# Performance work log

Measured on AMD Instinct MI355X. Metric: run time of the kernel, lower is better.

Reference implementation:

```python
import jax, jax.numpy as jnp
import numpy as np

B, S, D, V, K, H, L, U = 256, 50, 32, 10000, 16, 64, 2, 32
NORM = 0.01


def setup_inputs() -> dict:
    key = jax.random.key(0)
    ks = iter(jax.random.split(key, 64))
    r = lambda *sh: jax.random.normal(next(ks), sh, dtype=jnp.float32) * 0.05
    inp = {
        'x1': r(B, U), 'z1': r(B, S, D), 'x2': r(B, U), 'z2': r(B, S, D),
        'embd': r(V, D),
        'dec_w1': r(D, H), 'dec_b1': r(H), 'dec_w2': r(H, D), 'dec_b2': r(D),
        'i_wih': r(3 * D, D), 'i_whh': r(3 * D, D), 'i_bih': r(3 * D), 'i_bhh': r(3 * D),
        'c_wih': r(3 * D, D), 'c_whh': r(3 * D, D), 'c_bih': r(3 * D), 'c_bhh': r(3 * D),
        'im_w1': r(D, D), 'im_b1': r(D), 'im_w2': r(D, D), 'im_b2': r(D),
        'cm_w1': r(D, D), 'cm_b1': r(D), 'cm_w2': r(D, D), 'cm_b2': r(D),
        'hw1': r(L, D, K * K), 'hb1': r(L, K * K), 'hw2': r(L, D, K * K), 'hb2': r(L, K * K),
        'lin_w': r(L, U, K), 'lin_b': r(L, K), 'lout_w': r(L, K, U), 'lout_b': r(L, U),
        'sample_num': B, 'trigger_seq_length': 30,
    }
    return inp


def _gru(x, wih, whh, bih, bhh):
    # PyTorch GRU, batch_first, h0 = 0; gate order (r, z, n)
    gi = jnp.einsum('bsd,ed->bse', x, wih) + bih  # [B,S,3D]

    def step(h, gi_t):
        gh = h @ whh.T + bhh
        gir, giz, gin = jnp.split(gi_t, 3, axis=-1)
        ghr, ghz, ghn = jnp.split(gh, 3, axis=-1)
        rr = jax.nn.sigmoid(gir + ghr)
        zz = jax.nn.sigmoid(giz + ghz)
        nn = jnp.tanh(gin + rr * ghn)
        h = (1.0 - zz) * nn + zz * h
        return h, h

    h0 = jnp.zeros((x.shape[0], whh.shape[1]), x.dtype)
    _, hs = jax.lax.scan(step, h0, jnp.swapaxes(gi, 0, 1))
    return jnp.swapaxes(hs, 0, 1)  # [B,S,D]


def _forward(x1, z1, x2, z2, embd, dec_w1, dec_b1, dec_w2, dec_b2,
             i_wih, i_whh, i_bih, i_bhh, c_wih, c_whh, c_bih, c_bhh,
             im_w1, im_b1, im_w2, im_b2, cm_w1, cm_b1, cm_w2, cm_b2,
             hw1, hb1, hw2, hb2, lin_w, lin_b, lout_w, lout_b,
             sample_num, trigger_seq_length):
    # --- VQVAE.find_nearest: cdist + argmin + gather (index path has no grad) ---
    q = jax.lax.stop_gradient(z1)
    t = jax.lax.stop_gradient(embd)
    # ||q - t||^2 expanded; argmin over sqrt == argmin over squared dist
    d2 = ((q * q).sum(-1)[:, :, None]
          - 2.0 * jnp.einsum('bsd,vd->bsv', q, t)
          + (t * t).sum(-1)[None, None, :])  # [B,S,V]
    idx = jnp.argmin(d2, axis=2)  # [B,S]
    z_emb = embd[idx]  # [B,S,D], gradient flows into embd via gather

    # --- VQVAE.decode ---
    h = jax.nn.leaky_relu(z_emb @ dec_w1 + dec_b1, negative_slope=0.1)
    z_recon = h @ dec_w2 + dec_b2  # [B,S,D]

    total_loss = jnp.mean((z2 - jax.lax.stop_gradient(z_emb)) ** 2)

    # --- item branch: GRU -> pick trigger step -> MLP (tanh, linear) ---
    hs = _gru(z_recon, i_wih, i_whh, i_bih, i_bhh)
    u1 = hs[:, trigger_seq_length, :]
    z1f = jnp.tanh(u1 @ im_w1 + im_b1) @ im_w2 + im_b2  # [B,D]

    # --- category branch ---
    hs = _gru(z2, c_wih, c_whh, c_bih, c_bhh)
    u2 = hs[:, trigger_seq_length, :]
    z2f = jnp.tanh(u2 @ cm_w1 + cm_b1) @ cm_w2 + cm_b2  # [B,D]

    # --- hypernetwork layers (activations in self.modules are never applied) ---
    out = x1
    for i in range(L):
        iw = (z1f @ hw1[i] + hb1[i]).reshape(sample_num, K, K)
        cw = (z2f @ hw2[i] + hb2[i]).reshape(sample_num, K, K)
        w = jnp.clip(iw, -NORM, NORM) + cw  # [B,K,K]
        out = out @ lin_w[i] + lin_b[i]  # [B,K]
        out = jnp.einsum('bk,bkj->bj', out, w)  # bmm
        out = out @ lout_w[i] + lout_b[i]  # [B,U]
    return out, total_loss


def reference(x1, z1, x2, z2, embd, dec_w1, dec_b1, dec_w2, dec_b2,
              i_wih, i_whh, i_bih, i_bhh, c_wih, c_whh, c_bih, c_bhh,
              im_w1, im_b1, im_w2, im_b2, cm_w1, cm_b1, cm_w2, cm_b2,
              hw1, hb1, hw2, hb2, lin_w, lin_b, lout_w, lout_b,
              sample_num, trigger_seq_length):
    return _forward(x1, z1, x2, z2, embd, dec_w1, dec_b1, dec_w2, dec_b2,
                    i_wih, i_whh, i_bih, i_bhh, c_wih, c_whh, c_bih, c_bhh,
                    im_w1, im_b1, im_w2, im_b2, cm_w1, cm_b1, cm_w2, cm_b2,
                    hw1, hb1, hw2, hb2, lin_w, lin_b, lout_w, lout_b,
                    sample_num, trigger_seq_length)
```

## Files before the change

kernel.cpp:

```cpp
#include <hip/hip_runtime.h>
#include <math.h>

#define B 256
#define S 50
#define D 32
#define V 10000
#define VPAD 10240
#define KK 16
#define HH 64
#define LL 2
#define UU 32
#define TT 30
#define NROWS (B*S)
#define NORMC 0.01f
#define CH 256
#define NSLICE 8
#define SLICE_V 1280
#define VQ_RB 128

typedef __attribute__((ext_vector_type(8))) short bf16x8;
typedef __attribute__((ext_vector_type(4))) float f32x4;

__device__ __forceinline__ float sigmoidf_(float x) { return 1.0f / (1.0f + expf(-x)); }

__device__ __forceinline__ unsigned short f2bf(float x) {
    union { float f; unsigned int u; } a; a.f = x;
    unsigned int u = a.u;
    return (unsigned short)((u + 0x7FFFu + ((u >> 16) & 1u)) >> 16);
}
__device__ __forceinline__ float bf2f(unsigned short h) {
    union { unsigned int u; float f; } a; a.u = ((unsigned int)h) << 16; return a.f;
}

__device__ __forceinline__ void gld16(void* lds, const void* g) {
    __builtin_amdgcn_global_load_lds(
        (const __attribute__((address_space(1))) unsigned int*)g,
        (__attribute__((address_space(3))) unsigned int*)lds, 16, 0, 0);
}
__device__ __forceinline__ void gld4(void* lds, const void* g) {
    __builtin_amdgcn_global_load_lds(
        (const __attribute__((address_space(1))) unsigned int*)g,
        (__attribute__((address_space(3))) unsigned int*)lds, 4, 0, 0);
}

__global__ __launch_bounds__(256) void k_prep(const float* __restrict__ embd,
                                              const float* __restrict__ z1,
                                              unsigned short* __restrict__ Eh, unsigned short* __restrict__ El,
                                              unsigned short* __restrict__ Qh, unsigned short* __restrict__ Ql,
                                              float* __restrict__ tn, float* __restrict__ loss_sum) {
    int gid = blockIdx.x * 256 + threadIdx.x;
    if (gid == 0) loss_sum[0] = 0.f;
    if (gid >= VPAD * 4 + 4 * NROWS) return;
    int isRow = (gid >= VPAD * 4);
    if (!isRow) {
        int item = gid >> 2, qd = gid & 3;
        unsigned short* dh = Eh + (size_t)item * D + qd * 8;
        unsigned short* dl = El + (size_t)item * D + qd * 8;
        if (item >= V) {
            unsigned short z[8] = {0, 0, 0, 0, 0, 0, 0, 0};
            *(uint4*)dh = *(const uint4*)z;
            *(uint4*)dl = *(const uint4*)z;
            if (qd == 0) tn[item] = INFINITY;
            return;
        }
        const float* src = embd + (size_t)item * D + qd * 8;
        float4 x0 = *(const float4*)(src);
        float4 x1 = *(const float4*)(src + 4);
        float xs[8] = {x0.x, x0.y, x0.z, x0.w, x1.x, x1.y, x1.z, x1.w};
        unsigned short hv[8], lv[8];
        float ss = 0.f;
#pragma unroll
        for (int i = 0; i < 8; i++) {
            float x = xs[i];
            ss = fmaf(x, x, ss);
            unsigned short h = f2bf(x);
            hv[i] = h;
            lv[i] = f2bf(x - bf2f(h));
        }
        *(uint4*)dh = *(const uint4*)hv;
        *(uint4*)dl = *(const uint4*)lv;
        ss += __shfl_xor(ss, 1);
        ss += __shfl_xor(ss, 2);
        if (qd == 0) tn[item] = 0.5f * ss;
    } else {
        int g = gid - VPAD * 4;
        int item = g >> 2, qd = g & 3;
        const float* src = z1 + (size_t)item * D + qd * 8;
        unsigned short* dh = Qh + (size_t)item * D + qd * 8;
        unsigned short* dl = Ql + (size_t)item * D + qd * 8;
        float4 x0 = *(const float4*)(src);
        float4 x1 = *(const float4*)(src + 4);
        float xs[8] = {x0.x, x0.y, x0.z, x0.w, x1.x, x1.y, x1.z, x1.w};
        unsigned short hv[8], lv[8];
#pragma unroll
        for (int i = 0; i < 8; i++) {
            float x = -xs[i];
            unsigned short h = f2bf(x);
            hv[i] = h;
            lv[i] = f2bf(x - bf2f(h));
        }
        *(uint4*)dh = *(const uint4*)hv;
        *(uint4*)dl = *(const uint4*)lv;
    }
}

__global__ __launch_bounds__(256) void k_vq(const short* __restrict__ Qh, const short* __restrict__ Ql,
                                            const short* __restrict__ Eh, const short* __restrict__ El,
                                            const float* __restrict__ tn,
                                            float* __restrict__ pb_s, int* __restrict__ pb_v) {
    __shared__ __attribute__((aligned(16))) short EhL[CH * 32];
    __shared__ __attribute__((aligned(16))) short ElL[CH * 32];
    __shared__ float tnL[CH];
    const int tid = threadIdx.x;
    const int wave = tid >> 6, lane = tid & 63;
    const int rg = blockIdx.x >> 3, slice = blockIdx.x & 7;
    const int row0 = rg * VQ_RB;
    const int quad = lane >> 4, c15 = lane & 15;
    const int swz = quad ^ ((c15 >> 1) & 3);
    const int ar0 = row0 + wave * 32 + c15;
    bf16x8 ah0 = *(const bf16x8*)(Qh + (size_t)ar0 * 32 + quad * 8);
    bf16x8 al0 = *(const bf16x8*)(Ql + (size_t)ar0 * 32 + quad * 8);
    bf16x8 ah1 = *(const bf16x8*)(Qh + (size_t)(ar0 + 16) * 32 + quad * 8);
    bf16x8 al1 = *(const bf16x8*)(Ql + (size_t)(ar0 + 16) * 32 + quad * 8);
    float best0[4], best1[4]; int bv0[4], bv1[4];
#pragma unroll
    for (int i = 0; i < 4; i++) {
        best0[i] = INFINITY; best1[i] = INFINITY;
        bv0[i] = 0x7fffffff; bv1[i] = 0x7fffffff;
    }
    const int vbeg = slice * SLICE_V;
    for (int c0 = 0; c0 < SLICE_V; c0 += CH) {
        __syncthreads();
        {
            const int sbS = (vbeg + c0) * 32;
#pragma unroll
            for (int i = 0; i < 4; i++) {
                int c = wave * 256 + i * 64 + lane;
                int code = c >> 2;
                int q = (c & 3) ^ ((c >> 3) & 3);
                int srcOff = sbS + code * 32 + q * 8;
                int dstOff = (wave * 256 + i * 64) * 8;
                gld16(EhL + dstOff, Eh + srcOff);
                gld16(ElL + dstOff, El + srcOff);
            }
            gld4(tnL + wave * 64, tn + vbeg + c0 + wave * 64 + lane);
        }
        __syncthreads();
#pragma unroll
        for (int t = 0; t < 16; t++) {
            const int code = t * 16 + c15;
            const int boff = code * 32 + swz * 8;
            bf16x8 bh = *(const bf16x8*)(EhL + boff);
            bf16x8 bl = *(const bf16x8*)(ElL + boff);
            const float tnv = tnL[code];
            f32x4 acc0 = {tnv, tnv, tnv, tnv};
            f32x4 acc1 = {tnv, tnv, tnv, tnv};
            acc0 = __builtin_amdgcn_mfma_f32_16x16x32_bf16(ah0, bh, acc0, 0, 0, 0);
            acc1 = __builtin_amdgcn_mfma_f32_16x16x32_bf16(ah1, bh, acc1, 0, 0, 0);
            acc0 = __builtin_amdgcn_mfma_f32_16x16x32_bf16(al0, bh, acc0, 0, 0, 0);
            acc1 = __builtin_amdgcn_mfma_f32_16x16x32_bf16(al1, bh, acc1, 0, 0, 0);
            acc0 = __builtin_amdgcn_mfma_f32_16x16x32_bf16(ah0, bl, acc0, 0, 0, 0);
            acc1 = __builtin_amdgcn_mfma_f32_16x16x32_bf16(ah1, bl, acc1, 0, 0, 0);
            acc0 = __builtin_amdgcn_mfma_f32_16x16x32_bf16(al0, bl, acc0, 0, 0, 0);
            acc1 = __builtin_amdgcn_mfma_f32_16x16x32_bf16(al1, bl, acc1, 0, 0, 0);
            const int v = vbeg + c0 + code;
#pragma unroll
            for (int i = 0; i < 4; i++) {
                float s0 = acc0[i];
                if (s0 < best0[i]) { best0[i] = s0; bv0[i] = v; }
                float s1 = acc1[i];
                if (s1 < best1[i]) { best1[i] = s1; bv1[i] = v; }
            }
        }
    }
#pragma unroll
    for (int m = 1; m <= 8; m <<= 1) {
#pragma unroll
        for (int i = 0; i < 4; i++) {
            float os = __shfl_xor(best0[i], m); int ov = __shfl_xor(bv0[i], m);
            if (os < best0[i] || (os == best0[i] && ov < bv0[i])) { best0[i] = os; bv0[i] = ov; }
            os = __shfl_xor(best1[i], m); ov = __shfl_xor(bv1[i], m);
            if (os < best1[i] || (os == best1[i] && ov < bv1[i])) { best1[i] = os; bv1[i] = ov; }
        }
    }
    if (c15 == 0) {
#pragma unroll
        for (int i = 0; i < 4; i++) {
            int r0 = row0 + wave * 32 + quad * 4 + i;
            pb_s[(size_t)r0 * NSLICE + slice] = best0[i];
            pb_v[(size_t)r0 * NSLICE + slice] = bv0[i];
            int r1 = r0 + 16;
            pb_s[(size_t)r1 * NSLICE + slice] = best1[i];
            pb_v[(size_t)r1 * NSLICE + slice] = bv1[i];
        }
    }
}

__global__ __launch_bounds__(256) void k_gather(const float* __restrict__ z2,
                                                const float* __restrict__ embd,
                                                const float* __restrict__ pb_s,
                                                const int* __restrict__ pb_v,
                                                const float* __restrict__ dw1,
                                                const float* __restrict__ db1,
                                                const float* __restrict__ dw2,
                                                const float* __restrict__ db2,
                                                float* __restrict__ z_recon,
                                                float* __restrict__ loss_sum) {
    __shared__ float dw1L[2048];
    __shared__ float dw2L[2048];
    __shared__ float db1L[64], db2L[32];
    __shared__ int   vidL[32];
    __shared__ float zeL[32][33];
    __shared__ float aL[32][65];
    const int tid = threadIdx.x;
    const int row0 = blockIdx.x * 32;
    for (int p = tid; p < 2048; p += 256) { dw1L[p] = dw1[p]; dw2L[p] = dw2[p]; }
    if (tid < 64) db1L[tid] = db1[tid];
    if (tid >= 64 && tid < 96) db2L[tid - 64] = db2[tid - 64];
    if (tid < 32) {
        const int r = row0 + tid;
        float bs = INFINITY; int bv = 0x7fffffff;
#pragma unroll
        for (int j = 0; j < NSLICE; j++) {
            float s = pb_s[(size_t)r * NSLICE + j];
            int   v = pb_v[(size_t)r * NSLICE + j];
            if (s < bs) { bs = s; bv = v; }
        }
        vidL[tid] = bv;
    }
    __syncthreads();
    const int r = tid >> 3, q = tid & 7;
    {
        float4 e4 = *(const float4*)(embd + (size_t)vidL[r] * D + q * 4);
        zeL[r][q * 4 + 0] = e4.x; zeL[r][q * 4 + 1] = e4.y;
        zeL[r][q * 4 + 2] = e4.z; zeL[r][q * 4 + 3] = e4.w;
    }
    __syncthreads();
    {
        const float* zp = z2 + (size_t)(row0 + r) * D + q * 4;
        float4 x4 = *(const float4*)zp;
        float d0 = x4.x - zeL[r][q * 4 + 0], d1 = x4.y - zeL[r][q * 4 + 1];
        float d2 = x4.z - zeL[r][q * 4 + 2], d3 = x4.w - zeL[r][q * 4 + 3];
        float ls = d0 * d0 + d1 * d1 + d2 * d2 + d3 * d3;
#pragma unroll
        for (int off = 32; off > 0; off >>= 1) ls += __shfl_down(ls, off);
        if ((tid & 63) == 0) atomicAdd(loss_sum, ls);
    }
    const int s = (row0 + r) % S;
    const bool dec = (s <= TT);
    if (dec) {
#pragma unroll
        for (int j = 0; j < 8; j++) {
            int h = q * 8 + j;
            float a = db1L[h];
#pragma unroll
            for (int d = 0; d < 32; d++) a = fmaf(zeL[r][d], dw1L[d * 64 + h], a);
            aL[r][h] = (a >= 0.f) ? a : 0.1f * a;
        }
    }
    __syncthreads();
    if (dec) {
        const int b = (row0 + r) / S;
        float zr[4];
#pragma unroll
        for (int dd = 0; dd < 4; dd++) zr[dd] = db2L[q * 4 + dd];
        for (int h = 0; h < 64; h++) {
            float av = aL[r][h];
#pragma unroll
            for (int dd = 0; dd < 4; dd++) zr[dd] = fmaf(av, dw2L[h * 32 + q * 4 + dd], zr[dd]);
        }
        float4 o4 = make_float4(zr[0], zr[1], zr[2], zr[3]);
        *(float4*)(z_recon + (size_t)b * ((TT + 1) * D) + s * D + q * 4) = o4;
    }
}

__global__ __launch_bounds__(128) void k_gru(const float* __restrict__ z_recon,
                                             const float* __restrict__ z2,
                                             const float* __restrict__ i_wih, const float* __restrict__ i_whh,
                                             const float* __restrict__ i_bih, const float* __restrict__ i_bhh,
                                             const float* __restrict__ c_wih, const float* __restrict__ c_whh,
                                             const float* __restrict__ c_bih, const float* __restrict__ c_bhh,
                                             const float* __restrict__ im_w1, const float* __restrict__ im_b1,
                                             const float* __restrict__ im_w2, const float* __restrict__ im_b2,
                                             const float* __restrict__ cm_w1, const float* __restrict__ cm_b1,
                                             const float* __restrict__ cm_w2, const float* __restrict__ cm_b2,
                                             float* __restrict__ z1f, float* __restrict__ z2f) {
    const int tid = threadIdx.x;
    const int which = blockIdx.x >> 8;
    const int b = blockIdx.x & 255;
    const float* x; int xstride;
    const float *wih, *whh, *bih, *bhh, *w1, *b1, *w2, *b2; float* zf;
    if (which == 0) { x = z_recon; xstride = (TT + 1) * D; wih = i_wih; whh = i_whh; bih = i_bih; bhh = i_bhh; w1 = im_w1; b1 = im_b1; w2 = im_w2; b2 = im_b2; zf = z1f; }
    else            { x = z2;      xstride = S * D;        wih = c_wih; whh = c_whh; bih = c_bih; bhh = c_bhh; w1 = cm_w1; b1 = cm_b1; w2 = cm_w2; b2 = cm_b2; zf = z2f; }
    __shared__ float wihT[32][97];
    __shared__ float whhT[32][97];
    __shared__ float gi[TT + 1][96];
    __shared__ float xs[TT + 1][32];
    __shared__ float hsh[2][32];
    __shared__ float gh[96];
    __shared__ float bh2[96];
    __shared__ float af[32];
    for (int p = tid; p < 96 * 32; p += 128) {
        int e = p >> 5, d = p & 31;
        wihT[d][e] = wih[p];
        whhT[d][e] = whh[p];
    }
    for (int p = tid; p < (TT + 1) * D; p += 128) xs[p >> 5][p & 31] = x[(size_t)b * xstride + p];
    if (tid < 96) bh2[tid] = bhh[tid];
    if (tid < 32) hsh[0][tid] = 0.f;
    __syncthreads();
    for (int p = tid; p < (TT + 1) * 96; p += 128) {
        int s = p / 96, e = p % 96;
        float g0 = bih[e], g1 = 0.f;
#pragma unroll
        for (int d = 0; d < 16; d++) g0 = fmaf(xs[s][d], wihT[d][e], g0);
#pragma unroll
        for (int d = 16; d < 32; d++) g1 = fmaf(xs[s][d], wihT[d][e], g1);
        gi[s][e] = g0 + g1;
    }
    __syncthreads();
    for (int t = 0; t <= TT; t++) {
        const int cur = t & 1;
        if (tid < 96) {
            float g0 = bh2[tid], g1 = 0.f;
#pragma unroll
            for (int d = 0; d < 16; d++) g0 = fmaf(hsh[cur][d], whhT[d][tid], g0);
#pragma unroll
            for (int d = 16; d < 32; d++) g1 = fmaf(hsh[cur][d], whhT[d][tid], g1);
            gh[tid] = g0 + g1;
        }
        __syncthreads();
        if (tid < 32) {
            float rr = sigmoidf_(gi[t][tid] + gh[tid]);
            float zz = sigmoidf_(gi[t][tid + 32] + gh[tid + 32]);
            float nn = tanhf(gi[t][tid + 64] + rr * gh[tid + 64]);
            hsh[1 - cur][tid] = (1.f - zz) * nn + zz * hsh[cur][tid];
        }
        __syncthreads();
    }
    if (tid < 32) {
        float a = b1[tid];
#pragma unroll
        for (int d = 0; d < 32; d++) a = fmaf(hsh[1][d], w1[d * 32 + tid], a);
        af[tid] = tanhf(a);
    }
    __syncthreads();
    if (tid < 32) {
        float o = b2[tid];
#pragma unroll
        for (int d = 0; d < 32; d++) o = fmaf(af[d], w2[d * 32 + tid], o);
        zf[(size_t)b * 32 + tid] = o;
    }
}

__global__ __launch_bounds__(256) void k_wgen(const float* __restrict__ z1f_, const float* __restrict__ z2f_,
                                              const float* __restrict__ hw1, const float* __restrict__ hb1,
                                              const float* __restrict__ hw2, const float* __restrict__ hb2,
                                              float* __restrict__ w_out) {
    __shared__ float z1s[32], z2s[32];
    const int tid = threadIdx.x;
    const int b = blockIdx.x >> 1;
    const int layer = blockIdx.x & 1;
    if (tid < 32) z1s[tid] = z1f_[b * 32 + tid];
    else if (tid < 64) z2s[tid - 32] = z2f_[b * 32 + tid - 32];
    __syncthreads();
    const int kk = tid;
    const float* h1 = hw1 + layer * 8192 + kk;
    const float* h2 = hw2 + layer * 8192 + kk;
    float a = hb1[layer * 256 + kk];
    float c = hb2[layer * 256 + kk];
#pragma unroll
    for (int d = 0; d < 32; d++) {
        a = fmaf(z1s[d], h1[d * 256], a);
        c = fmaf(z2s[d], h2[d * 256], c);
    }
    a = fminf(fmaxf(a, -NORMC), NORMC);
    w_out[(size_t)b * 512 + layer * 256 + kk] = a + c;
}

__global__ __launch_bounds__(256) void k_apply(const float* __restrict__ x1,
                                               const float* __restrict__ w_in,
                                               const float* __restrict__ lin_w, const float* __restrict__ lin_b,
                                               const float* __restrict__ lout_w, const float* __restrict__ lout_b,
                                               const float* __restrict__ loss_sum, float* __restrict__ out) {
    __shared__ float linw[1024], loutw[1024], linb[32], loutb[64];
    __shared__ float wL[8][512];
    __shared__ float oc[8][32], t1s[8][16], t2s[8][16];
    const int tid = threadIdx.x;
    const int b0 = blockIdx.x * 8;
    {
        for (int p = tid; p < 1024; p += 256) { linw[p] = lin_w[p]; loutw[p] = lout_w[p]; }
        if (tid < 32) linb[tid] = lin_b[tid];
        if (tid >= 32 && tid < 96) loutb[tid - 32] = lout_b[tid - 32];
        const float4* src = (const float4*)(w_in + (size_t)b0 * 512);
#pragma unroll
        for (int i = 0; i < 4; i++) {
            float4 v = src[tid + i * 256];
            ((float4*)&wL[0][0])[tid + i * 256] = v;
        }
        float v = x1[b0 * 32 + tid];
        oc[tid >> 5][tid & 31] = v;
    }
    __syncthreads();
    const int s = tid >> 5, l = tid & 31;
#pragma unroll
    for (int i = 0; i < LL; i++) {
        if (l < 16) {
            float a = linb[i * 16 + l];
#pragma unroll
            for (int u = 0; u < 32; u++) a = fmaf(oc[s][u], linw[i * 512 + u * 16 + l], a);
            t1s[s][l] = a;
        }
        __syncthreads();
        if (l < 16) {
            float a = 0.f;
#pragma unroll
            for (int k = 0; k < 16; k++) a = fmaf(t1s[s][k], wL[s][i * 256 + k * 16 + l], a);
            t2s[s][l] = a;
        }
        __syncthreads();
        {
            float a = loutb[i * 32 + l];
#pragma unroll
            for (int k = 0; k < 16; k++) a = fmaf(t2s[s][k], loutw[i * 512 + k * 32 + l], a);
            oc[s][l] = a;
        }
        __syncthreads();
    }
    out[(size_t)(b0 + s) * 32 + l] = oc[s][l];
    if (blockIdx.x == 0 && tid == 0) out[B * UU] = loss_sum[0] * (1.0f / (float)(B * S * D));
}

extern "C" void kernel_launch(void* const* d_in, const int* in_sizes, int n_in,
                              void* d_out, int out_size, void* d_ws, size_t ws_size,
                              hipStream_t stream) {
    const float* x1     = (const float*)d_in[0];
    const float* z1     = (const float*)d_in[1];
    const float* z2     = (const float*)d_in[3];
    const float* embd   = (const float*)d_in[4];
    const float* dec_w1 = (const float*)d_in[5];
    const float* dec_b1 = (const float*)d_in[6];
    const float* dec_w2 = (const float*)d_in[7];
    const float* dec_b2 = (const float*)d_in[8];
    const float* i_wih  = (const float*)d_in[9];
    const float* i_whh  = (const float*)d_in[10];
    const float* i_bih  = (const float*)d_in[11];
    const float* i_bhh  = (const float*)d_in[12];
    const float* c_wih  = (const float*)d_in[13];
    const float* c_whh  = (const float*)d_in[14];
    const float* c_bih  = (const float*)d_in[15];
    const float* c_bhh  = (const float*)d_in[16];
    const float* im_w1  = (const float*)d_in[17];
    const float* im_b1  = (const float*)d_in[18];
    const float* im_w2  = (const float*)d_in[19];
    const float* im_b2  = (const float*)d_in[20];
    const float* cm_w1  = (const float*)d_in[21];
    const float* cm_b1  = (const float*)d_in[22];
    const float* cm_w2  = (const float*)d_in[23];
    const float* cm_b2  = (const float*)d_in[24];
    const float* hw1    = (const float*)d_in[25];
    const float* hb1    = (const float*)d_in[26];
    const float* hw2    = (const float*)d_in[27];
    const float* hb2    = (const float*)d_in[28];
    const float* lin_w  = (const float*)d_in[29];
    const float* lin_b  = (const float*)d_in[30];
    const float* lout_w = (const float*)d_in[31];
    const float* lout_b = (const float*)d_in[32];

    float* wsf      = (float*)d_ws;
    float* loss_sum = wsf;
    float* tn       = wsf + 64;
    float* pb_s     = wsf + 10304;
    int*   pb_v     = (int*)(wsf + 112704);
    unsigned short* Eh = (unsigned short*)(wsf + 215104);
    unsigned short* El = (unsigned short*)(wsf + 378944);
    unsigned short* Qh = (unsigned short*)(wsf + 542784);
    unsigned short* Ql = (unsigned short*)(wsf + 747584);
    float* z1f      = wsf + 952384;
    float* z2f      = wsf + 960576;
    float* z_recon  = (float*)Eh;
    float* w_out    = (float*)Qh;

    k_prep<<<(VPAD * 4 + 4 * NROWS + 255) / 256, 256, 0, stream>>>(embd, z1, Eh, El, Qh, Ql, tn, loss_sum);
    k_vq<<<(NROWS / VQ_RB) * NSLICE, 256, 0, stream>>>((const short*)Qh, (const short*)Ql,
                                                       (const short*)Eh, (const short*)El, tn, pb_s, pb_v);
    k_gather<<<NROWS / 32, 256, 0, stream>>>(z2, embd, pb_s, pb_v, dec_w1, dec_b1,
                                             dec_w2, dec_b2, z_recon, loss_sum);
    k_gru<<<512, 128, 0, stream>>>(z_recon, z2, i_wih, i_whh, i_bih, i_bhh,
                                   c_wih, c_whh, c_bih, c_bhh,
                                   im_w1, im_b1, im_w2, im_b2,
                                   cm_w1, cm_b1, cm_w2, cm_b2, z1f, z2f);
    k_wgen<<<2 * B, 256, 0, stream>>>(z1f, z2f, hw1, hb1, hw2, hb2, w_out);
    k_apply<<<B / 8, 256, 0, stream>>>(x1, w_out, lin_w, lin_b, lout_w, lout_b,
                                       loss_sum, (float*)d_out);
}
```

Measured before the change: 245.6 us.

## Fuse gather, GRU, hypernet and apply into one per-sample kernel; trim VQ MFMAs

Merges the gather/decoder, both GRUs, the hypernetwork weight generation and the apply stage into a single kernel with one block per sample. Both GRUs run concurrently inside that block, weights are held in registers, and a completion counter lets the last block write the loss. The VQ kernel now uses 10 slices of 1024 codes instead of 8, adds an occupancy hint, packs score and index into one float2, and drops the low-by-low MFMA correction term. This removes several launches and intermediate global buffers, at the cost of slightly lower distance precision (possible argmin ties flipping) and a long serial GRU inside each of only 256 blocks.

```diff
diff --git a/kernel.cpp b/kernel.cpp
--- a/kernel.cpp
+++ b/kernel.cpp
@@ -14,8 +14,8 @@
 #define NROWS (B*S)
 #define NORMC 0.01f
 #define CH 256
-#define NSLICE 8
-#define SLICE_V 1280
+#define NSLICE 10
+#define SLICE_V 1024
 #define VQ_RB 128
 
 typedef __attribute__((ext_vector_type(8))) short bf16x8;
@@ -47,9 +47,11 @@
                                               const float* __restrict__ z1,
                                               unsigned short* __restrict__ Eh, unsigned short* __restrict__ El,
                                               unsigned short* __restrict__ Qh, unsigned short* __restrict__ Ql,
-                                              float* __restrict__ tn, float* __restrict__ loss_sum) {
+                                              float* __restrict__ tn, float* __restrict__ loss_sum,
+                                              unsigned int* __restrict__ cnt) {
     int gid = blockIdx.x * 256 + threadIdx.x;
     if (gid == 0) loss_sum[0] = 0.f;
+    if (gid == 1) cnt[0] = 0u;
     if (gid >= VPAD * 4 + 4 * NROWS) return;
     int isRow = (gid >= VPAD * 4);
     if (!isRow) {
@@ -104,16 +106,16 @@
     }
 }
 
-__global__ __launch_bounds__(256) void k_vq(const short* __restrict__ Qh, const short* __restrict__ Ql,
-                                            const short* __restrict__ Eh, const short* __restrict__ El,
-                                            const float* __restrict__ tn,
-                                            float* __restrict__ pb_s, int* __restrict__ pb_v) {
+__global__ __launch_bounds__(256, 4) void k_vq(const short* __restrict__ Qh, const short* __restrict__ Ql,
+                                               const short* __restrict__ Eh, const short* __restrict__ El,
+                                               const float* __restrict__ tn,
+                                               float2* __restrict__ pbsv) {
     __shared__ __attribute__((aligned(16))) short EhL[CH * 32];
     __shared__ __attribute__((aligned(16))) short ElL[CH * 32];
     __shared__ float tnL[CH];
     const int tid = threadIdx.x;
     const int wave = tid >> 6, lane = tid & 63;
-    const int rg = blockIdx.x >> 3, slice = blockIdx.x & 7;
+    const int rg = blockIdx.x / NSLICE, slice = blockIdx.x % NSLICE;
     const int row0 = rg * VQ_RB;
     const int quad = lane >> 4, c15 = lane & 15;
     const int swz = quad ^ ((c15 >> 1) & 3);
@@ -161,8 +163,6 @@
             acc1 = __builtin_amdgcn_mfma_f32_16x16x32_bf16(al1, bh, acc1, 0, 0, 0);
             acc0 = __builtin_amdgcn_mfma_f32_16x16x32_bf16(ah0, bl, acc0, 0, 0, 0);
             acc1 = __builtin_amdgcn_mfma_f32_16x16x32_bf16(ah1, bl, acc1, 0, 0, 0);
-            acc0 = __builtin_amdgcn_mfma_f32_16x16x32_bf16(al0, bl, acc0, 0, 0, 0);
-            acc1 = __builtin_amdgcn_mfma_f32_16x16x32_bf16(al1, bl, acc1, 0, 0, 0);
             const int v = vbeg + c0 + code;
 #pragma unroll
             for (int i = 0; i < 4; i++) {
@@ -187,248 +187,274 @@
 #pragma unroll
         for (int i = 0; i < 4; i++) {
             int r0 = row0 + wave * 32 + quad * 4 + i;
-            pb_s[(size_t)r0 * NSLICE + slice] = best0[i];
-            pb_v[(size_t)r0 * NSLICE + slice] = bv0[i];
+            float2 p0; p0.x = best0[i]; p0.y = __int_as_float(bv0[i]);
+            pbsv[(size_t)r0 * NSLICE + slice] = p0;
             int r1 = r0 + 16;
-            pb_s[(size_t)r1 * NSLICE + slice] = best1[i];
-            pb_v[(size_t)r1 * NSLICE + slice] = bv1[i];
-        }
-    }
-}
-
-__global__ __launch_bounds__(256) void k_gather(const float* __restrict__ z2,
-                                                const float* __restrict__ embd,
-                                                const float* __restrict__ pb_s,
-                                                const int* __restrict__ pb_v,
-                                                const float* __restrict__ dw1,
-                                                const float* __restrict__ db1,
-                                                const float* __restrict__ dw2,
-                                                const float* __restrict__ db2,
-                                                float* __restrict__ z_recon,
-                                                float* __restrict__ loss_sum) {
-    __shared__ float dw1L[2048];
-    __shared__ float dw2L[2048];
+            float2 p1; p1.x = best1[i]; p1.y = __int_as_float(bv1[i]);
+            pbsv[(size_t)r1 * NSLICE + slice] = p1;
+        }
+    }
+}
+
+__global__ __launch_bounds__(256) void k_fused(
+        const float* __restrict__ x1, const float* __restrict__ z2,
+        const float* __restrict__ embd, const float2* __restrict__ pbsv,
+        const float* __restrict__ dw1, const float* __restrict__ db1,
+        const float* __restrict__ dw2, const float* __restrict__ db2,
+        const float* __restrict__ i_wih, const float* __restrict__ i_whh,
+        const float* __restrict__ i_bih, const float* __restrict__ i_bhh,
+        const float* __restrict__ c_wih, const float* __restrict__ c_whh,
+        const float* __restrict__ c_bih, const float* __restrict__ c_bhh,
+        const float* __restrict__ im_w1, const float* __restrict__ im_b1,
+        const float* __restrict__ im_w2, const float* __restrict__ im_b2,
+        const float* __restrict__ cm_w1, const float* __restrict__ cm_b1,
+        const float* __restrict__ cm_w2, const float* __restrict__ cm_b2,
+        const float* __restrict__ hw1, const float* __restrict__ hb1,
+        const float* __restrict__ hw2, const float* __restrict__ hb2,
+        const float* __restrict__ lin_w, const float* __restrict__ lin_b,
+        const float* __restrict__ lout_w, const float* __restrict__ lout_b,
+        float* __restrict__ loss_sum, unsigned int* __restrict__ cnt,
+        float* __restrict__ out) {
+    __shared__ float zeL[50][33];
+    __shared__ float dw1L[2048], dw2L[2048];
     __shared__ float db1L[64], db2L[32];
-    __shared__ int   vidL[32];
-    __shared__ float zeL[32][33];
-    __shared__ float aL[32][65];
+    __shared__ __attribute__((aligned(16))) float xsi[TT + 1][32];
+    __shared__ float gii[TT + 1][96], gic[TT + 1][96];
+    __shared__ float aL[TT + 1][65];
+    __shared__ __attribute__((aligned(16))) float hI[2][32], hC[2][32];
+    __shared__ float ghI[96], ghC[96];
+    __shared__ float afL[2][32];
+    __shared__ float z1fL[32], z2fL[32];
+    __shared__ float wW[512];
+    __shared__ float t1s[16], t2s[16], ocs[32];
+    __shared__ int   vidL[50];
+    __shared__ float lossRed[4];
     const int tid = threadIdx.x;
-    const int row0 = blockIdx.x * 32;
+    const int b = blockIdx.x;
+    const float* z2b = z2 + (size_t)b * (S * D);
+
     for (int p = tid; p < 2048; p += 256) { dw1L[p] = dw1[p]; dw2L[p] = dw2[p]; }
     if (tid < 64) db1L[tid] = db1[tid];
     if (tid >= 64 && tid < 96) db2L[tid - 64] = db2[tid - 64];
-    if (tid < 32) {
-        const int r = row0 + tid;
+    if (tid < 50) {
+        const float2* pp = pbsv + (size_t)(b * S + tid) * NSLICE;
         float bs = INFINITY; int bv = 0x7fffffff;
 #pragma unroll
         for (int j = 0; j < NSLICE; j++) {
-            float s = pb_s[(size_t)r * NSLICE + j];
-            int   v = pb_v[(size_t)r * NSLICE + j];
-            if (s < bs) { bs = s; bv = v; }
+            float2 p = pp[j];
+            int v = __float_as_int(p.y);
+            if (p.x < bs) { bs = p.x; bv = v; }
         }
         vidL[tid] = bv;
     }
     __syncthreads();
-    const int r = tid >> 3, q = tid & 7;
     {
-        float4 e4 = *(const float4*)(embd + (size_t)vidL[r] * D + q * 4);
-        zeL[r][q * 4 + 0] = e4.x; zeL[r][q * 4 + 1] = e4.y;
-        zeL[r][q * 4 + 2] = e4.z; zeL[r][q * 4 + 3] = e4.w;
+        const int q = tid & 7;
+#pragma unroll
+        for (int it = 0; it < 2; it++) {
+            int s = it * 32 + (tid >> 3);
+            if (s < 50) {
+                float4 e4 = *(const float4*)(embd + (size_t)vidL[s] * D + q * 4);
+                zeL[s][q * 4 + 0] = e4.x; zeL[s][q * 4 + 1] = e4.y;
+                zeL[s][q * 4 + 2] = e4.z; zeL[s][q * 4 + 3] = e4.w;
+            }
+        }
     }
     __syncthreads();
     {
-        const float* zp = z2 + (size_t)(row0 + r) * D + q * 4;
-        float4 x4 = *(const float4*)zp;
-        float d0 = x4.x - zeL[r][q * 4 + 0], d1 = x4.y - zeL[r][q * 4 + 1];
-        float d2 = x4.z - zeL[r][q * 4 + 2], d3 = x4.w - zeL[r][q * 4 + 3];
-        float ls = d0 * d0 + d1 * d1 + d2 * d2 + d3 * d3;
+        const int q = tid & 7;
+        float ls = 0.f;
+#pragma unroll
+        for (int it = 0; it < 2; it++) {
+            int s = it * 32 + (tid >> 3);
+            if (s < 50) {
+                float4 x4 = *(const float4*)(z2b + s * D + q * 4);
+                float d0 = x4.x - zeL[s][q * 4 + 0], d1 = x4.y - zeL[s][q * 4 + 1];
+                float d2 = x4.z - zeL[s][q * 4 + 2], d3 = x4.w - zeL[s][q * 4 + 3];
+                ls += d0 * d0 + d1 * d1 + d2 * d2 + d3 * d3;
+            }
+        }
 #pragma unroll
         for (int off = 32; off > 0; off >>= 1) ls += __shfl_down(ls, off);
-        if ((tid & 63) == 0) atomicAdd(loss_sum, ls);
-    }
-    const int s = (row0 + r) % S;
-    const bool dec = (s <= TT);
-    if (dec) {
-#pragma unroll
-        for (int j = 0; j < 8; j++) {
-            int h = q * 8 + j;
-            float a = db1L[h];
-#pragma unroll
-            for (int d = 0; d < 32; d++) a = fmaf(zeL[r][d], dw1L[d * 64 + h], a);
-            aL[r][h] = (a >= 0.f) ? a : 0.1f * a;
-        }
-    }
-    __syncthreads();
-    if (dec) {
-        const int b = (row0 + r) / S;
-        float zr[4];
-#pragma unroll
-        for (int dd = 0; dd < 4; dd++) zr[dd] = db2L[q * 4 + dd];
-        for (int h = 0; h < 64; h++) {
-            float av = aL[r][h];
-#pragma unroll
-            for (int dd = 0; dd < 4; dd++) zr[dd] = fmaf(av, dw2L[h * 32 + q * 4 + dd], zr[dd]);
-        }
-        float4 o4 = make_float4(zr[0], zr[1], zr[2], zr[3]);
-        *(float4*)(z_recon + (size_t)b * ((TT + 1) * D) + s * D + q * 4) = o4;
-    }
-}
-
-__global__ __launch_bounds__(128) void k_gru(const float* __restrict__ z_recon,
-                                             const float* __restrict__ z2,
-                                             const float* __restrict__ i_wih, const float* __restrict__ i_whh,
-                                             const float* __restrict__ i_bih, const float* __restrict__ i_bhh,
-                                             const float* __restrict__ c_wih, const float* __restrict__ c_whh,
-                                             const float* __restrict__ c_bih, const float* __restrict__ c_bhh,
-                                             const float* __restrict__ im_w1, const float* __restrict__ im_b1,
-                                             const float* __restrict__ im_w2, const float* __restrict__ im_b2,
-                                             const float* __restrict__ cm_w1, const float* __restrict__ cm_b1,
-                                             const float* __restrict__ cm_w2, const float* __restrict__ cm_b2,
-                                             float* __restrict__ z1f, float* __restrict__ z2f) {
-    const int tid = threadIdx.x;
-    const int which = blockIdx.x >> 8;
-    const int b = blockIdx.x & 255;
-    const float* x; int xstride;
-    const float *wih, *whh, *bih, *bhh, *w1, *b1, *w2, *b2; float* zf;
-    if (which == 0) { x = z_recon; xstride = (TT + 1) * D; wih = i_wih; whh = i_whh; bih = i_bih; bhh = i_bhh; w1 = im_w1; b1 = im_b1; w2 = im_w2; b2 = im_b2; zf = z1f; }
-    else            { x = z2;      xstride = S * D;        wih = c_wih; whh = c_whh; bih = c_bih; bhh = c_bhh; w1 = cm_w1; b1 = cm_b1; w2 = cm_w2; b2 = cm_b2; zf = z2f; }
-    __shared__ float wihT[32][97];
-    __shared__ float whhT[32][97];
-    __shared__ float gi[TT + 1][96];
-    __shared__ float xs[TT + 1][32];
-    __shared__ float hsh[2][32];
-    __shared__ float gh[96];
-    __shared__ float bh2[96];
-    __shared__ float af[32];
-    for (int p = tid; p < 96 * 32; p += 128) {
-        int e = p >> 5, d = p & 31;
-        wihT[d][e] = wih[p];
-        whhT[d][e] = whh[p];
-    }
-    for (int p = tid; p < (TT + 1) * D; p += 128) xs[p >> 5][p & 31] = x[(size_t)b * xstride + p];
-    if (tid < 96) bh2[tid] = bhh[tid];
-    if (tid < 32) hsh[0][tid] = 0.f;
-    __syncthreads();
-    for (int p = tid; p < (TT + 1) * 96; p += 128) {
-        int s = p / 96, e = p % 96;
-        float g0 = bih[e], g1 = 0.f;
-#pragma unroll
-        for (int d = 0; d < 16; d++) g0 = fmaf(xs[s][d], wihT[d][e], g0);
-#pragma unroll
-        for (int d = 16; d < 32; d++) g1 = fmaf(xs[s][d], wihT[d][e], g1);
-        gi[s][e] = g0 + g1;
-    }
+        if ((tid & 63) == 0) lossRed[tid >> 6] = ls;
+        const int s = tid >> 3;
+        if (s <= TT) {
+#pragma unroll
+            for (int j = 0; j < 8; j++) {
+                int h = q * 8 + j;
+                float a = db1L[h];
+#pragma unroll
+                for (int d = 0; d < 32; d++) a = fmaf(zeL[s][d], dw1L[d * 64 + h], a);
+                aL[s][h] = (a >= 0.f) ? a : 0.1f * a;
+            }
+        }
+    }
+    __syncthreads();
+    if (tid == 0) atomicAdd(loss_sum, lossRed[0] + lossRed[1] + lossRed[2] + lossRed[3]);
+    {
+        const int s = tid >> 3, q = tid & 7;
+        if (s <= TT) {
+            float zr[4];
+#pragma unroll
+            for (int dd = 0; dd < 4; dd++) zr[dd] = db2L[q * 4 + dd];
+            for (int h = 0; h < 64; h++) {
+                float av = aL[s][h];
+#pragma unroll
+                for (int dd = 0; dd < 4; dd++) zr[dd] = fmaf(av, dw2L[h * 32 + q * 4 + dd], zr[dd]);
+            }
+            float4 o4 = make_float4(zr[0], zr[1], zr[2], zr[3]);
+            *(float4*)&xsi[s][q * 4] = o4;
+        }
+    }
+    __syncthreads();
+    const bool actG = (tid < 96) || (tid >= 128 && tid < 224);
+    const int gru = (tid >= 128) ? 1 : 0;
+    const int e = gru ? (tid - 128) : tid;
+    if (actG) {
+        float wihRow[32];
+        const float* wg = gru ? c_wih : i_wih;
+#pragma unroll
+        for (int d = 0; d < 32; d++) wihRow[d] = wg[e * 32 + d];
+        const float bi = (gru ? c_bih : i_bih)[e];
+        float* giP = gru ? &gic[0][0] : &gii[0][0];
+        for (int s = 0; s <= TT; s++) {
+            float g = bi;
+            if (gru) {
+                const float4* xp = (const float4*)(z2b + s * D);
+#pragma unroll
+                for (int k = 0; k < 8; k++) {
+                    float4 xv = xp[k];
+                    g = fmaf(xv.x, wihRow[4 * k + 0], g);
+                    g = fmaf(xv.y, wihRow[4 * k + 1], g);
+                    g = fmaf(xv.z, wihRow[4 * k + 2], g);
+                    g = fmaf(xv.w, wihRow[4 * k + 3], g);
+                }
+            } else {
+                const float4* xp = (const float4*)&xsi[s][0];
+#pragma unroll
+                for (int k = 0; k < 8; k++) {
+                    float4 xv = xp[k];
+                    g = fmaf(xv.x, wihRow[4 * k + 0], g);
+                    g = fmaf(xv.y, wihRow[4 * k + 1], g);
+                    g = fmaf(xv.z, wihRow[4 * k + 2], g);
+                    g = fmaf(xv.w, wihRow[4 * k + 3], g);
+                }
+            }
+            giP[s * 96 + e] = g;
+        }
+    }
+    float whhRow[32]; float bh = 0.f;
+    if (actG) {
+        const float* wg = gru ? c_whh : i_whh;
+#pragma unroll
+        for (int d = 0; d < 32; d++) whhRow[d] = wg[e * 32 + d];
+        bh = (gru ? c_bhh : i_bhh)[e];
+    }
+    if (tid < 64) { (tid < 32 ? hI[0] : hC[0])[tid & 31] = 0.f; }
     __syncthreads();
     for (int t = 0; t <= TT; t++) {
         const int cur = t & 1;
-        if (tid < 96) {
-            float g0 = bh2[tid], g1 = 0.f;
-#pragma unroll
-            for (int d = 0; d < 16; d++) g0 = fmaf(hsh[cur][d], whhT[d][tid], g0);
-#pragma unroll
-            for (int d = 16; d < 32; d++) g1 = fmaf(hsh[cur][d], whhT[d][tid], g1);
-            gh[tid] = g0 + g1;
+        if (actG) {
+            float g = bh;
+            const float4* hp = (const float4*)(gru ? &hC[cur][0] : &hI[cur][0]);
+#pragma unroll
+            for (int k = 0; k < 8; k++) {
+                float4 hv = hp[k];
+                g = fmaf(hv.x, whhRow[4 * k + 0], g);
+                g = fmaf(hv.y, whhRow[4 * k + 1], g);
+                g = fmaf(hv.z, whhRow[4 * k + 2], g);
+                g = fmaf(hv.w, whhRow[4 * k + 3], g);
+            }
+            (gru ? ghC : ghI)[e] = g;
+        }
+        __syncthreads();
+        if (tid < 64) {
+            const int g2 = tid >> 5, l = tid & 31;
+            const float* giP = g2 ? &gic[t][0] : &gii[t][0];
+            const float* ghP = g2 ? ghC : ghI;
+            float* hP = g2 ? &hC[0][0] : &hI[0][0];
+            float rr = sigmoidf_(giP[l] + ghP[l]);
+            float zz = sigmoidf_(giP[l + 32] + ghP[l + 32]);
+            float nn = tanhf(giP[l + 64] + rr * ghP[l + 64]);
+            hP[(1 - cur) * 32 + l] = (1.f - zz) * nn + zz * hP[cur * 32 + l];
+        }
+        __syncthreads();
+    }
+    {
+        const bool actM = (tid < 32) || (tid >= 128 && tid < 160);
+        const int g2 = (tid >= 128) ? 1 : 0;
+        const int l = tid & 31;
+        if (actM) {
+            const float* w1 = g2 ? cm_w1 : im_w1;
+            const float* b1 = g2 ? cm_b1 : im_b1;
+            const float* hP = g2 ? &hC[1][0] : &hI[1][0];
+            float a = b1[l];
+#pragma unroll
+            for (int d = 0; d < 32; d++) a = fmaf(hP[d], w1[d * 32 + l], a);
+            afL[g2][l] = tanhf(a);
+        }
+        __syncthreads();
+        if (actM) {
+            const float* w2 = g2 ? cm_w2 : im_w2;
+            const float* b2 = g2 ? cm_b2 : im_b2;
+            float o = b2[l];
+#pragma unroll
+            for (int d = 0; d < 32; d++) o = fmaf(afL[g2][d], w2[d * 32 + l], o);
+            (g2 ? z2fL : z1fL)[l] = o;
+        }
+        if (tid < 32) ocs[tid] = x1[b * 32 + tid];
+    }
+    __syncthreads();
+    {
+        const int kk = tid;
+#pragma unroll
+        for (int ly = 0; ly < LL; ly++) {
+            float a = hb1[ly * 256 + kk], c = hb2[ly * 256 + kk];
+            const float* h1 = hw1 + ly * 8192 + kk;
+            const float* h2 = hw2 + ly * 8192 + kk;
+#pragma unroll
+            for (int d = 0; d < 32; d++) {
+                a = fmaf(z1fL[d], h1[d * 256], a);
+                c = fmaf(z2fL[d], h2[d * 256], c);
+            }
+            a = fminf(fmaxf(a, -NORMC), NORMC);
+            wW[ly * 256 + kk] = a + c;
+        }
+    }
+    __syncthreads();
+#pragma unroll
+    for (int i = 0; i < LL; i++) {
+        if (tid < 16) {
+            float a = lin_b[i * 16 + tid];
+#pragma unroll
+            for (int u = 0; u < 32; u++) a = fmaf(ocs[u], lin_w[i * 512 + u * 16 + tid], a);
+            t1s[tid] = a;
+        }
+        __syncthreads();
+        if (tid < 16) {
+            float a = 0.f;
+#pragma unroll
+            for (int k = 0; k < 16; k++) a = fmaf(t1s[k], wW[i * 256 + k * 16 + tid], a);
+            t2s[tid] = a;
         }
         __syncthreads();
         if (tid < 32) {
-            float rr = sigmoidf_(gi[t][tid] + gh[tid]);
-            float zz = sigmoidf_(gi[t][tid + 32] + gh[tid + 32]);
-            float nn = tanhf(gi[t][tid + 64] + rr * gh[tid + 64]);
-            hsh[1 - cur][tid] = (1.f - zz) * nn + zz * hsh[cur][tid];
-        }
-        __syncthreads();
-    }
-    if (tid < 32) {
-        float a = b1[tid];
-#pragma unroll
-        for (int d = 0; d < 32; d++) a = fmaf(hsh[1][d], w1[d * 32 + tid], a);
-        af[tid] = tanhf(a);
-    }
-    __syncthreads();
-    if (tid < 32) {
-        float o = b2[tid];
-#pragma unroll
-        for (int d = 0; d < 32; d++) o = fmaf(af[d], w2[d * 32 + tid], o);
-        zf[(size_t)b * 32 + tid] = o;
-    }
-}
-
-__global__ __launch_bounds__(256) void k_wgen(const float* __restrict__ z1f_, const float* __restrict__ z2f_,
-                                              const float* __restrict__ hw1, const float* __restrict__ hb1,
-                                              const float* __restrict__ hw2, const float* __restrict__ hb2,
-                                              float* __restrict__ w_out) {
-    __shared__ float z1s[32], z2s[32];
-    const int tid = threadIdx.x;
-    const int b = blockIdx.x >> 1;
-    const int layer = blockIdx.x & 1;
-    if (tid < 32) z1s[tid] = z1f_[b * 32 + tid];
-    else if (tid < 64) z2s[tid - 32] = z2f_[b * 32 + tid - 32];
-    __syncthreads();
-    const int kk = tid;
-    const float* h1 = hw1 + layer * 8192 + kk;
-    const float* h2 = hw2 + layer * 8192 + kk;
-    float a = hb1[layer * 256 + kk];
-    float c = hb2[layer * 256 + kk];
-#pragma unroll
-    for (int d = 0; d < 32; d++) {
-        a = fmaf(z1s[d], h1[d * 256], a);
-        c = fmaf(z2s[d], h2[d * 256], c);
-    }
-    a = fminf(fmaxf(a, -NORMC), NORMC);
-    w_out[(size_t)b * 512 + layer * 256 + kk] = a + c;
-}
-
-__global__ __launch_bounds__(256) void k_apply(const float* __restrict__ x1,
-                                               const float* __restrict__ w_in,
-                                               const float* __restrict__ lin_w, const float* __restrict__ lin_b,
-                                               const float* __restrict__ lout_w, const float* __restrict__ lout_b,
-                                               const float* __restrict__ loss_sum, float* __restrict__ out) {
-    __shared__ float linw[1024], loutw[1024], linb[32], loutb[64];
-    __shared__ float wL[8][512];
-    __shared__ float oc[8][32], t1s[8][16], t2s[8][16];
-    const int tid = threadIdx.x;
-    const int b0 = blockIdx.x * 8;
-    {
-        for (int p = tid; p < 1024; p += 256) { linw[p] = lin_w[p]; loutw[p] = lout_w[p]; }
-        if (tid < 32) linb[tid] = lin_b[tid];
-        if (tid >= 32 && tid < 96) loutb[tid - 32] = lout_b[tid - 32];
-        const float4* src = (const float4*)(w_in + (size_t)b0 * 512);
-#pragma unroll
-        for (int i = 0; i < 4; i++) {
-            float4 v = src[tid + i * 256];
-            ((float4*)&wL[0][0])[tid + i * 256] = v;
-        }
-        float v = x1[b0 * 32 + tid];
-        oc[tid >> 5][tid & 31] = v;
-    }
-    __syncthreads();
-    const int s = tid >> 5, l = tid & 31;
-#pragma unroll
-    for (int i = 0; i < LL; i++) {
-        if (l < 16) {
-            float a = linb[i * 16 + l];
-#pragma unroll
-            for (int u = 0; u < 32; u++) a = fmaf(oc[s][u], linw[i * 512 + u * 16 + l], a);
-            t1s[s][l] = a;
-        }
-        __syncthreads();
-        if (l < 16) {
-            float a = 0.f;
-#pragma unroll
-            for (int k = 0; k < 16; k++) a = fmaf(t1s[s][k], wL[s][i * 256 + k * 16 + l], a);
-            t2s[s][l] = a;
-        }
-        __syncthreads();
-        {
-            float a = loutb[i * 32 + l];
-#pragma unroll
-            for (int k = 0; k < 16; k++) a = fmaf(t2s[s][k], loutw[i * 512 + k * 32 + l], a);
-            oc[s][l] = a;
-        }
-        __syncthreads();
-    }
-    out[(size_t)(b0 + s) * 32 + l] = oc[s][l];
-    if (blockIdx.x == 0 && tid == 0) out[B * UU] = loss_sum[0] * (1.0f / (float)(B * S * D));
+            float a = lout_b[i * 32 + tid];
+#pragma unroll
+            for (int k = 0; k < 16; k++) a = fmaf(t2s[k], lout_w[i * 512 + k * 32 + tid], a);
+            ocs[tid] = a;
+        }
+        __syncthreads();
+    }
+    if (tid < 32) out[(size_t)b * 32 + tid] = ocs[tid];
+    if (tid == 0) {
+        __threadfence();
+        unsigned int old = atomicAdd(cnt, 1u);
+        if (old == B - 1) {
+            float tot = atomicAdd(loss_sum, 0.0f);
+            out[B * UU] = tot * (1.0f / (float)(B * S * D));
+        }
+    }
 }
 
 extern "C" void kernel_launch(void* const* d_in, const int* in_sizes, int n_in,
@@ -469,28 +495,25 @@
 
     float* wsf      = (float*)d_ws;
     float* loss_sum = wsf;
+    unsigned int* cnt = (unsigned int*)(wsf + 1);
     float* tn       = wsf + 64;
-    float* pb_s     = wsf + 10304;
-    int*   pb_v     = (int*)(wsf + 112704);
-    unsigned short* Eh = (unsigned short*)(wsf + 215104);
-    unsigned short* El = (unsigned short*)(wsf + 378944);
-    unsigned short* Qh = (unsigned short*)(wsf + 542784);
-    unsigned short* Ql = (unsigned short*)(wsf + 747584);
-    float* z1f      = wsf + 952384;
-    float* z2f      = wsf + 960576;
-    float* z_recon  = (float*)Eh;
-    float* w_out    = (float*)Qh;
-
-    k_prep<<<(VPAD * 4 + 4 * NROWS + 255) / 256, 256, 0, stream>>>(embd, z1, Eh, El, Qh, Ql, tn, loss_sum);
+    float2* pbsv    = (float2*)(wsf + 10304);
+    unsigned short* Eh = (unsigned short*)(wsf + 266304);
+    unsigned short* El = (unsigned short*)(wsf + 430144);
+    unsigned short* Qh = (unsigned short*)(wsf + 593984);
+    unsigned short* Ql = (unsigned short*)(wsf + 798784);
+
+    k_prep<<<(VPAD * 4 + 4 * NROWS + 255) / 256, 256, 0, stream>>>(embd, z1, Eh, El, Qh, Ql,
+                                                                   tn, loss_sum, cnt);
     k_vq<<<(NROWS / VQ_RB) * NSLICE, 256, 0, stream>>>((const short*)Qh, (const short*)Ql,
-                                                       (const short*)Eh, (const short*)El, tn, pb_s, pb_v);
-    k_gather<<<NROWS / 32, 256, 0, stream>>>(z2, embd, pb_s, pb_v, dec_w1, dec_b1,
-                                             dec_w2, dec_b2, z_recon, loss_sum);
-    k_gru<<<512, 128, 0, stream>>>(z_recon, z2, i_wih, i_whh, i_bih, i_bhh,
+                                                       (const short*)Eh, (const short*)El, tn, pbsv);
+    k_fused<<<B, 256, 0, stream>>>(x1, z2, embd, pbsv,
+                                   dec_w1, dec_b1, dec_w2, dec_b2,
+                                   i_wih, i_whh, i_bih, i_bhh,
                                    c_wih, c_whh, c_bih, c_bhh,
                                    im_w1, im_b1, im_w2, im_b2,
-                                   cm_w1, cm_b1, cm_w2, cm_b2, z1f, z2f);
-    k_wgen<<<2 * B, 256, 0, stream>>>(z1f, z2f, hw1, hb1, hw2, hb2, w_out);
-    k_apply<<<B / 8, 256, 0, stream>>>(x1, w_out, lin_w, lin_b, lout_w, lout_b,
-                                       loss_sum, (float*)d_out);
-}
+                                   cm_w1, cm_b1, cm_w2, cm_b2,
+                                   hw1, hb1, hw2, hb2,
+                                   lin_w, lin_b, lout_w, lout_b,
+                                   loss_sum, cnt, (float*)d_out);
+}
```

After: 196.7 us. -19.9%, faster.
